# Optimization experiments

Hardware: AMD Instinct MI355X
Metric: run time of the kernel (lower is better)

## Reference

```python
import jax, jax.numpy as jnp
import numpy as np

N_NODES = 50000
N_EDGES = 800000
IN_CH = 256
OUT_CH = 64
HEADS = 4


def setup_inputs() -> dict:
    key = jax.random.key(0)
    k1, k2, k3, k4, k5 = jax.random.split(key, 5)
    x = jax.random.normal(k1, (N_NODES, IN_CH), dtype=jnp.float32)
    edge_index = jax.random.randint(k2, (2, N_EDGES), 0, N_NODES, dtype=jnp.int64)
    # xavier-ish scaled params
    weight = jax.random.normal(k3, (HEADS, IN_CH, OUT_CH), dtype=jnp.float32) * (2.0 / (IN_CH + OUT_CH)) ** 0.5
    att_src = jax.random.normal(k4, (1, HEADS, OUT_CH), dtype=jnp.float32) * 0.1
    att_dst = jax.random.normal(k5, (1, HEADS, OUT_CH), dtype=jnp.float32) * 0.1
    bias = jnp.zeros((HEADS * OUT_CH,), dtype=jnp.float32)
    return {"x": x, "edge_index": edge_index, "weight": weight,
            "att_src": att_src, "att_dst": att_dst, "bias": bias}


def reference(x, edge_index, weight, att_src, att_dst, bias):
    # GATConv forward (eval mode: dropout is identity), vectorized over heads.
    num_nodes = x.shape[0]
    row, col = edge_index[0], edge_index[1]
    # per-head projection: [N, H, C]
    x_h = jnp.einsum('nf,hfc->nhc', x, weight)
    alpha_src = jnp.sum(x_h * att_src[0], axis=-1)   # [N, H]
    alpha_dst = jnp.sum(x_h * att_dst[0], axis=-1)   # [N, H]
    alpha = alpha_src[row] + alpha_dst[col]          # [E, H]
    alpha = jax.nn.leaky_relu(alpha, negative_slope=0.2)
    # segment softmax over edges grouped by destination row (numerically stable)
    alpha_max = jax.ops.segment_max(alpha, row, num_segments=num_nodes)  # [N, H]
    alpha = jnp.exp(alpha - alpha_max[row])
    alpha_sum = jax.ops.segment_sum(alpha, row, num_segments=num_nodes)  # [N, H]
    alpha = alpha / jnp.clip(alpha_sum[row], 1e-16)
    # message passing: scatter-add alpha-weighted source features
    messages = alpha[:, :, None] * x_h[col]                              # [E, H, C]
    out = jax.ops.segment_sum(messages, row, num_segments=num_nodes)    # [N, H, C]
    out = out.reshape(num_nodes, -1) + bias                              # concat heads
    return out
```

## Files before the change

### kernel.cpp

```cpp
#include <hip/hip_runtime.h>
#include <hip/hip_fp16.h>
#include <math.h>

#define N_IN_CH 256
#define N_OUT   256
#define HEADS   4
#define OUT_CH  64
#define BM      64
#define HM      32
#define NSLOT   16
#define SCAN_BLOCK 1024

typedef __attribute__((ext_vector_type(8))) short bf16x8;
typedef __attribute__((ext_vector_type(4))) float f32x4;

__device__ __forceinline__ float lrelu(float a) {
  return a >= 0.f ? a : 0.2f * a;
}

__device__ __forceinline__ ushort f2bf(float f) {
  uint u = __float_as_uint(f);
  uint r = (u + 0x7FFFu + ((u >> 16) & 1u)) >> 16;
  return (ushort)r;
}

__device__ __forceinline__ ushort f2h(float f) {
  return __half_as_ushort(__float2half(f));
}
__device__ __forceinline__ float h2f(ushort u) {
  return __half2float(__ushort_as_half(u));
}

__device__ __forceinline__ int wave_scan_partials(const int* __restrict__ partials,
                                                  int nparts, int lane) {
  int pv = (lane < nparts) ? partials[lane] : 0;
  int incl = pv;
#pragma unroll
  for (int d = 1; d < 64; d <<= 1) {
    int t = __shfl_up(incl, d, 64);
    if (lane >= d) incl += t;
  }
  return incl - pv;
}

__global__ void convert_w(const float* __restrict__ w, ushort* __restrict__ bt) {
  const int idx = blockIdx.x * 256 + threadIdx.x;
  const int n = idx >> 8, k = idx & 255;
  const int h = n >> 6, c = n & 63;
  bt[idx] = f2bf(w[h * (N_IN_CH * OUT_CH) + k * OUT_CH + c]);
}

__global__ __launch_bounds__(256) void proj_count(
    const float* __restrict__ x, const ushort* __restrict__ bt,
    const float* __restrict__ att_src, const float* __restrict__ att_dst,
    ushort* __restrict__ xh, float* __restrict__ asrc, float* __restrict__ adst,
    int nnodes, int nblocksA,
    const int* __restrict__ row, int* __restrict__ hist,
    int* __restrict__ rank, int nedges) {
  __shared__ ushort at[HM * N_IN_CH];
  const int tid = threadIdx.x;
  const int bid = blockIdx.x;
  const int g = bid / 5;
  const bool is_proj = (bid % 5 == 0) && (g < nblocksA);

  if (!is_proj) {
    const int cb = (bid % 5 == 0) ? (4 * g)
                                  : (4 * g + (bid % 5) - 1);
    const int e = cb * 256 + tid;
    if (e < nedges)
      rank[e] = atomicAdd(&hist[(e & (NSLOT - 1)) * nnodes + row[e]], 1);
    return;
  }

  const int wave = tid >> 6;
  const int lane = tid & 63;
  const int lmod = lane & 15;
  const int ldiv = lane >> 4;

  float atts[4], attd[4];
#pragma unroll
  for (int nt = 0; nt < 4; ++nt) {
    const int gcol = wave * 64 + nt * 16 + lmod;
    atts[nt] = att_src[gcol];
    attd[nt] = att_dst[gcol];
  }

  for (int h0 = 0; h0 < 2; ++h0) {
    const int n0 = g * BM + h0 * HM;

    {
      const int rsub = tid >> 6;
      const int cf = (tid & 63) * 4;
      const int cb2 = cf * 2;
#pragma unroll
      for (int it = 0; it < 8; ++it) {
        const int lr = it * 4 + rsub;
        const int grow = n0 + lr;
        float4 xv = make_float4(0.f, 0.f, 0.f, 0.f);
        if (grow < nnodes) xv = *(const float4*)&x[(size_t)grow * N_IN_CH + cf];
        ushort4 b;
        b.x = f2bf(xv.x); b.y = f2bf(xv.y); b.z = f2bf(xv.z); b.w = f2bf(xv.w);
        const int cbs = cb2 ^ ((lr & 7) << 4);
        *(ushort4*)((char*)at + lr * 512 + cbs) = b;
      }
    }
    __syncthreads();

    f32x4 acc[2][4];
#pragma unroll
    for (int mt = 0; mt < 2; ++mt)
#pragma unroll
      for (int nt = 0; nt < 4; ++nt) acc[mt][nt] = (f32x4){0.f, 0.f, 0.f, 0.f};

    for (int ks = 0; ks < 8; ++ks) {
      bf16x8 a[2], b[4];
#pragma unroll
      for (int mt = 0; mt < 2; ++mt) {
        const int lr = mt * 16 + lmod;
        const int kb = ks * 64 + ldiv * 16;
        const int cbs = kb ^ ((lr & 7) << 4);
        a[mt] = *(const bf16x8*)((const char*)at + lr * 512 + cbs);
      }
#pragma unroll
      for (int nt = 0; nt < 4; ++nt) {
        const int n = wave * 64 + nt * 16 + lmod;
        b[nt] = *(const bf16x8*)&bt[(size_t)n * N_IN_CH + ks * 32 + ldiv * 8];
      }
#pragma unroll
      for (int mt = 0; mt < 2; ++mt)
#pragma unroll
        for (int nt = 0; nt < 4; ++nt)
          acc[mt][nt] = __builtin_amdgcn_mfma_f32_16x16x32_bf16(
              a[mt], b[nt], acc[mt][nt], 0, 0, 0);
    }

#pragma unroll
    for (int mt = 0; mt < 2; ++mt) {
#pragma unroll
      for (int reg = 0; reg < 4; ++reg) {
        const int grow = n0 + mt * 16 + ldiv * 4 + reg;
        const bool ok = grow < nnodes;
        float vs = 0.f, vd = 0.f;
#pragma unroll
        for (int nt = 0; nt < 4; ++nt) {
          const float v = acc[mt][nt][reg];
          if (ok) xh[(size_t)grow * N_OUT + wave * 64 + nt * 16 + lmod] = f2h(v);
          vs = fmaf(v, atts[nt], vs);
          vd = fmaf(v, attd[nt], vd);
        }
#pragma unroll
        for (int d = 1; d < 16; d <<= 1) {
          vs += __shfl_xor(vs, d, 64);
          vd += __shfl_xor(vd, d, 64);
        }
        if (lmod == 0 && ok) {
          asrc[grow * HEADS + wave] = vs;
          adst[grow * HEADS + wave] = vd;
        }
      }
    }
    __syncthreads();
  }
}

__global__ __launch_bounds__(SCAN_BLOCK) void scan1_kernel(
    int* __restrict__ hist, int* __restrict__ offsets,
    int* __restrict__ partials, int n) {
  __shared__ int wsum[16];
  const int tid = threadIdx.x;
  const int lane = tid & 63;
  const int wid = tid >> 6;
  const int i = blockIdx.x * SCAN_BLOCK + tid;

  int v = 0;
  if (i < n) {
    int running = 0;
#pragma unroll
    for (int s = 0; s < NSLOT; ++s) {
      const int h = hist[s * n + i];
      hist[s * n + i] = running;
      running += h;
    }
    v = running;
  }

  int incl = v;
#pragma unroll
  for (int d = 1; d < 64; d <<= 1) {
    int t = __shfl_up(incl, d, 64);
    if (lane >= d) incl += t;
  }
  if (lane == 63) wsum[wid] = incl;
  __syncthreads();
  if (wid == 0) {
    int wv = (lane < 16) ? wsum[lane] : 0;
#pragma unroll
    for (int d = 1; d < 16; d <<= 1) {
      int t = __shfl_up(wv, d, 64);
      if (lane >= d) wv += t;
    }
    if (lane < 16) wsum[lane] = wv;
  }
  __syncthreads();
  const int wexcl = (wid == 0) ? 0 : wsum[wid - 1];
  if (i <= n) offsets[i] = wexcl + incl - v;
  if (tid == SCAN_BLOCK - 1) partials[blockIdx.x] = wsum[15];
}

__global__ void scatter_kernel(const int* __restrict__ row, const int* __restrict__ col,
                               const int* __restrict__ rank,
                               const int* __restrict__ offsets,
                               const int* __restrict__ hist,
                               const int* __restrict__ partials, int nparts,
                               const float* __restrict__ asrc,
                               const float* __restrict__ adst,
                               uint4* __restrict__ erec, int nedges, int nnodes) {
  const int lane = threadIdx.x & 63;
  const int excl = wave_scan_partials(partials, nparts, lane);
  int e = blockIdx.x * blockDim.x + threadIdx.x;
  if (e < nedges) {
    const int r = row[e];
    const int c = col[e];
    const int pos = offsets[r] + __shfl(excl, r >> 10, 64) +
                    hist[(e & (NSLOT - 1)) * nnodes + r] + rank[e];
    const float4 s = *(const float4*)&asrc[r * 4];
    const float4 d = *(const float4*)&adst[c * 4];
    uint4 rec;
    rec.x = (uint)c;
    rec.y = (uint)f2h(__expf(lrelu(s.x + d.x))) |
            ((uint)f2h(__expf(lrelu(s.y + d.y))) << 16);
    rec.z = (uint)f2h(__expf(lrelu(s.z + d.z))) |
            ((uint)f2h(__expf(lrelu(s.w + d.w))) << 16);
    rec.w = 0u;
    erec[pos] = rec;
  }
}

__global__ __launch_bounds__(256) void gather_kernel(
    const int* __restrict__ offsets,
    const int* __restrict__ partials, int nparts,
    const uint4* __restrict__ erec,
    const ushort* __restrict__ xh, const float* __restrict__ bias,
    float* __restrict__ out, int nnodes) {
  __shared__ float pbuf[4][64 * 4];
  const int wv = threadIdx.x >> 6;
  const int lane = threadIdx.x & 63;
  const int n = blockIdx.x * 4 + wv;
  if (n >= nnodes) return;
  const int excl = wave_scan_partials(partials, nparts, lane);
  const int off = offsets[n] + __shfl(excl, n >> 10, 64);
  const int end = offsets[n + 1] + __shfl(excl, (n + 1) >> 10, 64);
  const int deg = end - off;
  const int half = lane >> 5;
  const int ch8 = (lane & 31) * 8;
  const int hh = (lane & 31) >> 3;

  float wsum = 0.f;
  float a0 = 0.f, a1 = 0.f, a2 = 0.f, a3 = 0.f;
  float a4 = 0.f, a5 = 0.f, a6 = 0.f, a7 = 0.f;

  for (int b = 0; b < deg; b += 64) {
    const int cnt = min(64, deg - b);
    int cl_l = 0;
    float4 p = make_float4(0.f, 0.f, 0.f, 0.f);
    if (lane < cnt) {
      const uint4 rec = erec[off + b + lane];
      cl_l = (int)rec.x;
      p.x = h2f((ushort)(rec.y & 0xFFFFu));
      p.y = h2f((ushort)(rec.y >> 16));
      p.z = h2f((ushort)(rec.z & 0xFFFFu));
      p.w = h2f((ushort)(rec.z >> 16));
    }
    *(float4*)&pbuf[wv][lane * 4] = p;

    for (int j = 0; j < cnt; j += 16) {
      int cq[8];
#pragma unroll
      for (int q = 0; q < 8; ++q) cq[q] = __shfl(cl_l, j + 2 * q + half, 64);
      uint4 xq[8];
#pragma unroll
      for (int q = 0; q < 8; ++q)
        xq[q] = *(const uint4*)&xh[(size_t)cq[q] * N_OUT + ch8];

      float wq[8];
#pragma unroll
      for (int q = 0; q < 8; ++q) wq[q] = pbuf[wv][(j + 2 * q + half) * 4 + hh];

#pragma unroll
      for (int q = 0; q < 8; ++q) {
        wsum += wq[q];
        a0 = fmaf(wq[q], h2f((ushort)(xq[q].x & 0xFFFFu)), a0);
        a1 = fmaf(wq[q], h2f((ushort)(xq[q].x >> 16)), a1);
        a2 = fmaf(wq[q], h2f((ushort)(xq[q].y & 0xFFFFu)), a2);
        a3 = fmaf(wq[q], h2f((ushort)(xq[q].y >> 16)), a3);
        a4 = fmaf(wq[q], h2f((ushort)(xq[q].z & 0xFFFFu)), a4);
        a5 = fmaf(wq[q], h2f((ushort)(xq[q].z >> 16)), a5);
        a6 = fmaf(wq[q], h2f((ushort)(xq[q].w & 0xFFFFu)), a6);
        a7 = fmaf(wq[q], h2f((ushort)(xq[q].w >> 16)), a7);
      }
    }
  }

  a0 += __shfl_xor(a0, 32, 64);
  a1 += __shfl_xor(a1, 32, 64);
  a2 += __shfl_xor(a2, 32, 64);
  a3 += __shfl_xor(a3, 32, 64);
  a4 += __shfl_xor(a4, 32, 64);
  a5 += __shfl_xor(a5, 32, 64);
  a6 += __shfl_xor(a6, 32, 64);
  a7 += __shfl_xor(a7, 32, 64);
  wsum += __shfl_xor(wsum, 32, 64);

  const float invh = 1.f / fmaxf(wsum, 1e-16f);

  const int wch = ch8 + half * 4;
  const float4 b4 = *(const float4*)&bias[wch];
  float4 o;
  o.x = fmaf(half ? a4 : a0, invh, b4.x);
  o.y = fmaf(half ? a5 : a1, invh, b4.y);
  o.z = fmaf(half ? a6 : a2, invh, b4.z);
  o.w = fmaf(half ? a7 : a3, invh, b4.w);
  *(float4*)&out[(size_t)n * N_OUT + wch] = o;
}

extern "C" void kernel_launch(void* const* d_in, const int* in_sizes, int n_in,
                              void* d_out, int out_size, void* d_ws, size_t ws_size,
                              hipStream_t stream) {
  const float* x        = (const float*)d_in[0];
  const int*   edge_idx = (const int*)d_in[1];
  const float* weight   = (const float*)d_in[2];
  const float* att_src  = (const float*)d_in[3];
  const float* att_dst  = (const float*)d_in[4];
  const float* bias     = (const float*)d_in[5];
  float* out = (float*)d_out;

  const int nnodes = in_sizes[0] / N_IN_CH;
  const int nedges = in_sizes[1] / 2;
  const int* row = edge_idx;
  const int* col = edge_idx + nedges;

  char* wsb = (char*)d_ws;
  size_t woff = 0;
  auto alloc = [&](size_t bytes) -> char* {
    char* p = wsb + woff;
    woff += (bytes + 255) & ~(size_t)255;
    return p;
  };
  ushort* xh    = (ushort*)alloc((size_t)nnodes * N_OUT * sizeof(ushort));
  ushort* bt    = (ushort*)alloc((size_t)N_OUT * N_IN_CH * sizeof(ushort));
  float* asrc   = (float*)alloc((size_t)nnodes * HEADS * sizeof(float));
  float* adst   = (float*)alloc((size_t)nnodes * HEADS * sizeof(float));
  int* hist     = (int*)alloc((size_t)nnodes * NSLOT * sizeof(int));
  int* offsets  = (int*)alloc((size_t)(nnodes + 1) * sizeof(int));
  int* partials = (int*)alloc(256 * sizeof(int));
  int* rank     = (int*)alloc((size_t)nedges * sizeof(int));
  uint4* erec   = (uint4*)alloc((size_t)nedges * sizeof(uint4));

  hipMemsetAsync(hist, 0, (size_t)nnodes * NSLOT * sizeof(int), stream);

  convert_w<<<256, 256, 0, stream>>>(weight, bt);

  const int eblocks = (nedges + 255) / 256;
  const int nblocksA = (nnodes + BM - 1) / BM;
  const int total = nblocksA + eblocks;
  proj_count<<<total, 256, 0, stream>>>(
      x, bt, att_src, att_dst, xh, asrc, adst, nnodes, nblocksA,
      row, hist, rank, nedges);

  const int nscan = (nnodes + 1 + SCAN_BLOCK - 1) / SCAN_BLOCK;
  scan1_kernel<<<nscan, SCAN_BLOCK, 0, stream>>>(hist, offsets, partials, nnodes);

  scatter_kernel<<<eblocks, 256, 0, stream>>>(row, col, rank, offsets, hist,
                                              partials, nscan,
                                              asrc, adst, erec, nedges, nnodes);

  gather_kernel<<<(nnodes + 3) / 4, 256, 0, stream>>>(offsets, partials, nscan,
                                                      erec, xh, bias, out, nnodes);
}
```

Before: 161.8 us.

## Partition degree-count atomics by XCD and fold histogram zeroing into convert_w

The per-edge degree-count atomics now go to one of 8 per-XCD histogram copies, chosen by reading the hardware XCC_ID register, instead of 16 slots picked by edge index. The atomic uses the sc0 scope hint inline, and the rank packs the XCD id into its high bits. The aim is to keep atomic contention local to each die's L2 and to halve the histogram size for scan and zeroing. The separate memset is dropped and the zeroing is folded into convert_w. Risks are the non-portable inline asm, a forced vmcnt(0) wait per atomic, a 16-bit rank limit, and correctness that depends on the memory scope of atomics hitting the same copy from one XCD.

```diff
diff --git a/kernel.cpp b/kernel.cpp
--- a/kernel.cpp
+++ b/kernel.cpp
@@ -8,7 +8,7 @@
 #define OUT_CH  64
 #define BM      64
 #define HM      32
-#define NSLOT   16
+#define NXCD    8
 #define SCAN_BLOCK 1024
 
 typedef __attribute__((ext_vector_type(8))) short bf16x8;
@@ -43,8 +43,13 @@
   return incl - pv;
 }
 
-__global__ void convert_w(const float* __restrict__ w, ushort* __restrict__ bt) {
+__global__ void convert_w(const float* __restrict__ w, ushort* __restrict__ bt,
+                          int* __restrict__ counts8, int nnodes) {
   const int idx = blockIdx.x * 256 + threadIdx.x;
+  if (idx < nnodes) {
+#pragma unroll
+    for (int s = 0; s < NXCD; ++s) counts8[s * nnodes + idx] = 0;
+  }
   const int n = idx >> 8, k = idx & 255;
   const int h = n >> 6, c = n & 63;
   bt[idx] = f2bf(w[h * (N_IN_CH * OUT_CH) + k * OUT_CH + c]);
@@ -55,7 +60,7 @@
     const float* __restrict__ att_src, const float* __restrict__ att_dst,
     ushort* __restrict__ xh, float* __restrict__ asrc, float* __restrict__ adst,
     int nnodes, int nblocksA,
-    const int* __restrict__ row, int* __restrict__ hist,
+    const int* __restrict__ row, int* __restrict__ counts8,
     int* __restrict__ rank, int nedges) {
   __shared__ ushort at[HM * N_IN_CH];
   const int tid = threadIdx.x;
@@ -67,8 +72,21 @@
     const int cb = (bid % 5 == 0) ? (4 * g)
                                   : (4 * g + (bid % 5) - 1);
     const int e = cb * 256 + tid;
-    if (e < nedges)
-      rank[e] = atomicAdd(&hist[(e & (NSLOT - 1)) * nnodes + row[e]], 1);
+    if (e < nedges) {
+      const int r = row[e];
+      uint xcc;
+      asm("s_getreg_b32 %0, hwreg(HW_REG_XCC_ID)" : "=s"(xcc));
+      xcc &= (NXCD - 1);
+      int* ap = &counts8[(size_t)xcc * nnodes + r];
+      int old;
+      asm volatile(
+          "global_atomic_add %0, %1, %2, off sc0\n\t"
+          "s_waitcnt vmcnt(0)"
+          : "=v"(old)
+          : "v"(ap), "v"(1)
+          : "memory");
+      rank[e] = (int)((xcc << 16) | (uint)old);
+    }
     return;
   }
 
@@ -164,7 +182,7 @@
 }
 
 __global__ __launch_bounds__(SCAN_BLOCK) void scan1_kernel(
-    int* __restrict__ hist, int* __restrict__ offsets,
+    int* __restrict__ counts8, int* __restrict__ offsets,
     int* __restrict__ partials, int n) {
   __shared__ int wsum[16];
   const int tid = threadIdx.x;
@@ -176,9 +194,9 @@
   if (i < n) {
     int running = 0;
 #pragma unroll
-    for (int s = 0; s < NSLOT; ++s) {
-      const int h = hist[s * n + i];
-      hist[s * n + i] = running;
+    for (int s = 0; s < NXCD; ++s) {
+      const int h = counts8[s * n + i];
+      counts8[s * n + i] = running;
       running += h;
     }
     v = running;
@@ -210,7 +228,7 @@
 __global__ void scatter_kernel(const int* __restrict__ row, const int* __restrict__ col,
                                const int* __restrict__ rank,
                                const int* __restrict__ offsets,
-                               const int* __restrict__ hist,
+                               const int* __restrict__ counts8,
                                const int* __restrict__ partials, int nparts,
                                const float* __restrict__ asrc,
                                const float* __restrict__ adst,
@@ -221,8 +239,10 @@
   if (e < nedges) {
     const int r = row[e];
     const int c = col[e];
+    const int rk = rank[e];
+    const int xcc = (rk >> 16) & (NXCD - 1);
     const int pos = offsets[r] + __shfl(excl, r >> 10, 64) +
-                    hist[(e & (NSLOT - 1)) * nnodes + r] + rank[e];
+                    counts8[(size_t)xcc * nnodes + r] + (rk & 0xFFFF);
     const float4 s = *(const float4*)&asrc[r * 4];
     const float4 d = *(const float4*)&adst[c * 4];
     uint4 rec;
@@ -350,27 +370,25 @@
   ushort* bt    = (ushort*)alloc((size_t)N_OUT * N_IN_CH * sizeof(ushort));
   float* asrc   = (float*)alloc((size_t)nnodes * HEADS * sizeof(float));
   float* adst   = (float*)alloc((size_t)nnodes * HEADS * sizeof(float));
-  int* hist     = (int*)alloc((size_t)nnodes * NSLOT * sizeof(int));
+  int* counts8  = (int*)alloc((size_t)nnodes * NXCD * sizeof(int));
   int* offsets  = (int*)alloc((size_t)(nnodes + 1) * sizeof(int));
   int* partials = (int*)alloc(256 * sizeof(int));
   int* rank     = (int*)alloc((size_t)nedges * sizeof(int));
   uint4* erec   = (uint4*)alloc((size_t)nedges * sizeof(uint4));
 
-  hipMemsetAsync(hist, 0, (size_t)nnodes * NSLOT * sizeof(int), stream);
-
-  convert_w<<<256, 256, 0, stream>>>(weight, bt);
+  convert_w<<<256, 256, 0, stream>>>(weight, bt, counts8, nnodes);
 
   const int eblocks = (nedges + 255) / 256;
   const int nblocksA = (nnodes + BM - 1) / BM;
   const int total = nblocksA + eblocks;
   proj_count<<<total, 256, 0, stream>>>(
       x, bt, att_src, att_dst, xh, asrc, adst, nnodes, nblocksA,
-      row, hist, rank, nedges);
+      row, counts8, rank, nedges);
 
   const int nscan = (nnodes + 1 + SCAN_BLOCK - 1) / SCAN_BLOCK;
-  scan1_kernel<<<nscan, SCAN_BLOCK, 0, stream>>>(hist, offsets, partials, nnodes);
-
-  scatter_kernel<<<eblocks, 256, 0, stream>>>(row, col, rank, offsets, hist,
+  scan1_kernel<<<nscan, SCAN_BLOCK, 0, stream>>>(counts8, offsets, partials, nnodes);
+
+  scatter_kernel<<<eblocks, 256, 0, stream>>>(row, col, rank, offsets, counts8,
                                               partials, nscan,
                                               asrc, adst, erec, nedges, nnodes);
 
```

Measured after the change: 154.5 us. 4.5% less time.
